# Kernel optimization log

Hardware: AMD Instinct MI355X
Metric: run time of the kernel (lower is better)

## Reference

```python
import jax, jax.numpy as jnp
import numpy as np

N, M, D = 8, 512, 64
B, H, W = 8192, 1, 1


def setup_inputs() -> dict:
    key = jax.random.key(0)
    k1, k2, k3 = jax.random.split(key, 3)
    x = jax.random.normal(k1, (B, N * D, H, W), dtype=jnp.float32)
    # nn.init.uniform_(embedding, -1/M, 1/M)
    embedding = jax.random.uniform(k2, (N, M, D), dtype=jnp.float32,
                                   minval=-1.0 / M, maxval=1.0 / M)
    # uniform base noise for Gumbel sampling (avoid exact 0)
    u = jax.random.uniform(k3, (N, B, H, W, M), dtype=jnp.float32,
                           minval=1e-6, maxval=1.0)
    tau = jnp.ones((1,), dtype=jnp.float32)
    return {"x": x, "embedding": embedding, "u": u, "tau": tau}


def reference(x, embedding, u, tau):
    n, m, d = embedding.shape
    b, c, h, w = x.shape
    # (B, N*D, H, W) -> (N, B*H*W, D)
    xr = x.reshape(b, n, d, h, w).transpose(1, 0, 3, 4, 2).reshape(n, b * h * w, d)
    e_sq = jnp.sum(embedding ** 2, axis=2)[:, None, :]          # (N, 1, M)
    x_sq = jnp.sum(xr ** 2, axis=2, keepdims=True)              # (N, BHW, 1)
    distances = e_sq + x_sq - 2.0 * jnp.einsum('nbd,nmd->nbm', xr, embedding)
    logits = -distances.reshape(n, b, h, w, m)
    # RelaxedOneHotCategorical normalizes logits to log-probs
    log_probs = jax.nn.log_softmax(logits, axis=-1)
    probs = jnp.exp(log_probs)
    # rsample: softmax((logits + gumbel) / tau); shift-invariant so log_probs ok
    gumbels = -jnp.log(-jnp.log(u))
    samples = jax.nn.softmax((log_probs + gumbels) / tau[0], axis=-1).reshape(n, -1, m)
    quantized = jnp.einsum('nbm,nmd->nbd', samples, embedding).reshape(n, b, 1, 1, d)
    logM = jnp.log(jnp.asarray(m, dtype=x.dtype))
    KL = jnp.where(probs == 0, jnp.zeros_like(probs), probs * (log_probs + logM))
    KL = KL.sum(axis=(0, 2, 3, 4)).mean()
    avg_probs = samples.mean(axis=1)                            # (N, M)
    perplexity = jnp.exp(-jnp.sum(avg_probs * jnp.log(avg_probs + 1e-10), axis=-1))
    ret_logits = jnp.transpose(log_probs, (1, 0, 4, 2, 3))      # (B, N, M, H, W)
    quantized = jnp.transpose(quantized, (1, 0, 4, 2, 3))       # (B, N, D, 1, 1)
    return (quantized, KL, perplexity.sum(), ret_logits)
```

## Files before the change

### kernel.cpp

```cpp
#include <hip/hip_runtime.h>
#include <stdint.h>

typedef short short8 __attribute__((ext_vector_type(8)));
typedef float float4v __attribute__((ext_vector_type(4)));
typedef unsigned long long ull;

#define R2      65536
#define LDS_SZ  81920

__device__ __forceinline__ unsigned cvtpk(float a, float b){
  unsigned d;
  asm("v_cvt_pk_bf16_f32 %0, %1, %2" : "=v"(d) : "v"(a), "v"(b));
  return d;
}
__device__ __forceinline__ unsigned short f2bf(float f){
  unsigned u = __float_as_uint(f);
  return (unsigned short)((u + 0x7FFFu + ((u >> 16) & 1u)) >> 16);
}

template<int OFF>
__device__ __forceinline__ ull tr16(unsigned a){
  ull d;
  asm volatile("ds_read_b64_tr_b16 %0, %1 offset:%c2" : "=v"(d) : "v"(a), "i"(OFF));
  return d;
}
__device__ __forceinline__ short8 mk8(ull lo, ull hi){
  union { ull q[2]; short8 v; } u; u.q[0] = lo; u.q[1] = hi; return u.v;
}

extern "C" __global__ void __launch_bounds__(512, 4)
vq_main(const float* __restrict__ gx, const float* __restrict__ ge,
        const float* __restrict__ gu, const float* __restrict__ gtau,
        float* __restrict__ gq, float* __restrict__ glg,
        float* __restrict__ ws_avg, float* __restrict__ ws_kl)
{
  extern __shared__ char smem[];
  const int tid = threadIdx.x;
  const int n   = blockIdx.x >> 6;
  const int b0  = (blockIdx.x & 63) * 128;

  float esq_reg = 0.f;
  {
    const int m = tid;
    const float* src = ge + (size_t)(n * 512 + m) * 64;
    char* dst = smem + m * 128;
    const unsigned sw = (unsigned)((m & 7) << 4);
#pragma unroll
    for (int c = 0; c < 8; ++c) {
      float4 a = *(const float4*)(src + c * 8);
      float4 b = *(const float4*)(src + c * 8 + 4);
      esq_reg += a.x*a.x + a.y*a.y + a.z*a.z + a.w*a.w
               + b.x*b.x + b.y*b.y + b.z*b.z + b.w*b.w;
      uint4 v = { cvtpk(a.x, a.y), cvtpk(a.z, a.w), cvtpk(b.x, b.y), cvtpk(b.z, b.w) };
      *(uint4*)(dst + (((unsigned)(c * 16)) ^ sw)) = v;
    }
  }
  {
    const int r = tid >> 2, qq = tid & 3;
    const float* src = gx + (size_t)(b0 + r) * 512 + n * 64 + qq * 16;
    char* dst = smem + R2 + r * 128;
    const unsigned sw = (unsigned)((r & 7) << 4);
#pragma unroll
    for (int h = 0; h < 2; ++h) {
      float4 a = *(const float4*)(src + h * 8);
      float4 b = *(const float4*)(src + h * 8 + 4);
      uint4 v = { cvtpk(a.x, a.y), cvtpk(a.z, a.w), cvtpk(b.x, b.y), cvtpk(b.z, b.w) };
      *(uint4*)(dst + (((unsigned)((qq * 2 + h) * 16)) ^ sw)) = v;
    }
  }
  __syncthreads();

  const int lane = tid & 63;
  const int w    = tid >> 6;
  const int l15  = lane & 15;
  const int kg   = lane >> 4;
  const unsigned swl = (unsigned)((l15 & 7) << 4);

  const char* xrow = smem + R2 + (w * 16 + l15) * 128;
  const short8 xb0 = *(const short8*)(xrow + (((unsigned)(kg * 16)) ^ swl));
  const short8 xb1 = *(const short8*)(xrow + (((unsigned)(64 + kg * 16)) ^ swl));
  __syncthreads();
  ((float*)(smem + R2))[tid] = esq_reg;
  __syncthreads();

  const char* erow = smem + l15 * 128;
  const unsigned eo0 = ((unsigned)(kg * 16)) ^ swl;
  const unsigned eo1 = ((unsigned)(64 + kg * 16)) ^ swl;
  const float* esqp = (const float*)(smem + R2);

  const float invtau = 1.0f / gtau[0];
  const float4* up4 = (const float4*)(gu + (size_t)n * 4194304
                     + (size_t)(b0 + w * 16 + l15) * 512 + kg * 4);

  float Z = 0.f, Wk = 0.f, Z2 = 0.f;
  {
    float4 Pa = up4[0], Pb = up4[4], Pc = up4[8], Pd = up4[12];
#pragma unroll
    for (int t = 0; t < 32; ++t) {
      short8 eb0 = *(const short8*)(erow + t * 2048 + eo0);
      short8 eb1 = *(const short8*)(erow + t * 2048 + eo1);
      float4v d = (float4v){0.f, 0.f, 0.f, 0.f};
      d = __builtin_amdgcn_mfma_f32_16x16x32_bf16(eb0, xb0, d, 0, 0, 0);
      d = __builtin_amdgcn_mfma_f32_16x16x32_bf16(eb1, xb1, d, 0, 0, 0);
      const float4 eq = *(const float4*)(esqp + t * 16 + kg * 4);
      const float s0 = 2.f * d[0] - eq.x;
      const float s1 = 2.f * d[1] - eq.y;
      const float s2 = 2.f * d[2] - eq.z;
      const float s3 = 2.f * d[3] - eq.w;
      const float e0 = __expf(s0), e1 = __expf(s1), e2 = __expf(s2), e3 = __expf(s3);
      Z  += e0 + e1 + e2 + e3;
      Wk += e0 * s0 + e1 * s1 + e2 * s2 + e3 * s3;
      const float4 uu = Pa;
      Pa = Pb; Pb = Pc; Pc = Pd;
      if (t < 28) Pd = up4[(t + 4) * 4];
      const float g0 = -__logf(-__logf(uu.x));
      const float g1 = -__logf(-__logf(uu.y));
      const float g2 = -__logf(-__logf(uu.z));
      const float g3 = -__logf(-__logf(uu.w));
      Z2 += __expf((s0 + g0) * invtau) + __expf((s1 + g1) * invtau)
          + __expf((s2 + g2) * invtau) + __expf((s3 + g3) * invtau);
    }
  }
  Z  += __shfl_xor(Z, 16);  Z  += __shfl_xor(Z, 32);
  Wk += __shfl_xor(Wk, 16); Wk += __shfl_xor(Wk, 32);
  Z2 += __shfl_xor(Z2, 16); Z2 += __shfl_xor(Z2, 32);
  const float lse = __logf(Z);
  const float logM = 6.2383246250395075f;
  float klrow = Wk / Z - lse + logM;
  const float rz2 = 1.0f / Z2;

  float4v* lp4 = (float4v*)(glg + (size_t)(b0 + w * 16 + l15) * 4096 + n * 512 + kg * 4);
  ushort* sampw = (ushort*)(smem + R2 + 8192 + w * 1024);
  const char* sampc = (const char*)sampw;
  const unsigned trA = (unsigned)(uintptr_t)sampw
                     + (unsigned)(kg * 128 + (l15 >> 2) * 32 + (l15 & 3) * 8);
  const int mrow = kg * 4 + (l15 >> 2);
  const unsigned ebase = (unsigned)(uintptr_t)smem + (unsigned)(mrow * 128);
  const unsigned msw = ((unsigned)(mrow & 7)) << 4;
  unsigned trB0 = ebase + ((unsigned)(  0 + (l15 & 3) * 8) ^ msw);
  unsigned trB1 = ebase + ((unsigned)( 32 + (l15 & 3) * 8) ^ msw);
  unsigned trB2 = ebase + ((unsigned)( 64 + (l15 & 3) * 8) ^ msw);
  unsigned trB3 = ebase + ((unsigned)( 96 + (l15 & 3) * 8) ^ msw);

  float4v qacc0 = (float4v){0.f,0.f,0.f,0.f};
  float4v qacc1 = (float4v){0.f,0.f,0.f,0.f};
  float4v qacc2 = (float4v){0.f,0.f,0.f,0.f};
  float4v qacc3 = (float4v){0.f,0.f,0.f,0.f};
  float4v avgA  = (float4v){0.f,0.f,0.f,0.f};
  float4v avgB  = (float4v){0.f,0.f,0.f,0.f};

  float4 P0 = up4[0], P1 = up4[4], P2 = up4[8], P3 = up4[12];
#pragma unroll
  for (int c = 0; c < 16; ++c) {
    const float4 cu0 = P0, cu1 = P1;
    P0 = P2; P1 = P3;
    if (c < 14) { P2 = up4[(2 * c + 4) * 4]; P3 = up4[(2 * c + 5) * 4]; }
#pragma unroll
    for (int th = 0; th < 2; ++th) {
      const int t = c * 2 + th;
      short8 eb0 = *(const short8*)(erow + t * 2048 + eo0);
      short8 eb1 = *(const short8*)(erow + t * 2048 + eo1);
      float4v d = (float4v){0.f, 0.f, 0.f, 0.f};
      d = __builtin_amdgcn_mfma_f32_16x16x32_bf16(eb0, xb0, d, 0, 0, 0);
      d = __builtin_amdgcn_mfma_f32_16x16x32_bf16(eb1, xb1, d, 0, 0, 0);
      const float4 eq = *(const float4*)(esqp + t * 16 + kg * 4);
      const float s0 = 2.f * d[0] - eq.x;
      const float s1 = 2.f * d[1] - eq.y;
      const float s2 = 2.f * d[2] - eq.z;
      const float s3 = 2.f * d[3] - eq.w;
      float4v lpv = { s0 - lse, s1 - lse, s2 - lse, s3 - lse };
      lp4[t * 4] = lpv;
      const float4 uu = (th == 0) ? cu0 : cu1;
      const float g0 = -__logf(-__logf(uu.x));
      const float g1 = -__logf(-__logf(uu.y));
      const float g2 = -__logf(-__logf(uu.z));
      const float g3 = -__logf(-__logf(uu.w));
      const float y0 = __expf((s0 + g0) * invtau) * rz2;
      const float y1 = __expf((s1 + g1) * invtau) * rz2;
      const float y2 = __expf((s2 + g2) * invtau) * rz2;
      const float y3 = __expf((s3 + g3) * invtau) * rz2;
      sampw[(th * 16 + kg * 4 + 0) * 16 + l15] = f2bf(y0);
      sampw[(th * 16 + kg * 4 + 1) * 16 + l15] = f2bf(y1);
      sampw[(th * 16 + kg * 4 + 2) * 16 + l15] = f2bf(y2);
      sampw[(th * 16 + kg * 4 + 3) * 16 + l15] = f2bf(y3);
    }
    asm volatile("s_waitcnt lgkmcnt(0)" ::: "memory");
    __builtin_amdgcn_sched_barrier(0);
    const short8 avA = *(const short8*)(sampc + l15 * 32 + (kg & 1) * 16);
    const short8 avB = *(const short8*)(sampc + 512 + l15 * 32 + (kg & 1) * 16);
    ull alo = tr16<0>(trA),  ahi = tr16<512>(trA);
    ull b0l = tr16<0>(trB0), b0h = tr16<2048>(trB0);
    ull b1l = tr16<0>(trB1), b1h = tr16<2048>(trB1);
    ull b2l = tr16<0>(trB2), b2h = tr16<2048>(trB2);
    ull b3l = tr16<0>(trB3), b3h = tr16<2048>(trB3);
    asm volatile("s_waitcnt lgkmcnt(0)" ::: "memory");
    __builtin_amdgcn_sched_barrier(0);
    const unsigned onv = ((l15 == c) && (kg < 2)) ? 0x3F803F80u : 0u;
    union { unsigned u[4]; short8 v; } bs;
    bs.u[0] = onv; bs.u[1] = onv; bs.u[2] = onv; bs.u[3] = onv;
    short8 aa = mk8(alo, ahi);
    qacc0 = __builtin_amdgcn_mfma_f32_16x16x32_bf16(aa, mk8(b0l, b0h), qacc0, 0, 0, 0);
    qacc1 = __builtin_amdgcn_mfma_f32_16x16x32_bf16(aa, mk8(b1l, b1h), qacc1, 0, 0, 0);
    qacc2 = __builtin_amdgcn_mfma_f32_16x16x32_bf16(aa, mk8(b2l, b2h), qacc2, 0, 0, 0);
    qacc3 = __builtin_amdgcn_mfma_f32_16x16x32_bf16(aa, mk8(b3l, b3h), qacc3, 0, 0, 0);
    avgA  = __builtin_amdgcn_mfma_f32_16x16x32_bf16(avA, bs.v, avgA, 0, 0, 0);
    avgB  = __builtin_amdgcn_mfma_f32_16x16x32_bf16(avB, bs.v, avgB, 0, 0, 0);
    trB0 += 4096; trB1 += 4096; trB2 += 4096; trB3 += 4096;
  }

  {
    const size_t qb = (size_t)(b0 + w * 16 + kg * 4) * 512 + n * 64 + l15;
#pragma unroll
    for (int j = 0; j < 4; ++j) {
      gq[qb + (size_t)j * 512 +  0] = qacc0[j];
      gq[qb + (size_t)j * 512 + 16] = qacc1[j];
      gq[qb + (size_t)j * 512 + 32] = qacc2[j];
      gq[qb + (size_t)j * 512 + 48] = qacc3[j];
    }
  }

  klrow += __shfl_xor(klrow, 1); klrow += __shfl_xor(klrow, 2);
  klrow += __shfl_xor(klrow, 4); klrow += __shfl_xor(klrow, 8);

  __syncthreads();
  float* avgl = (float*)(smem + R2);
  float* kls  = (float*)smem;
  if (lane == 0) kls[w] = klrow;
  *(float4v*)(avgl + w * 512 + l15 * 32 + kg * 4)      = avgA;
  *(float4v*)(avgl + w * 512 + l15 * 32 + 16 + kg * 4) = avgB;
  __syncthreads();
  {
    float s = 0.f;
#pragma unroll
    for (int ww = 0; ww < 8; ++ww) s += avgl[ww * 512 + tid];
    ws_avg[(size_t)blockIdx.x * 512 + tid] = s;
    if (tid == 0) {
      float k = 0.f;
#pragma unroll
      for (int i = 0; i < 8; ++i) k += kls[i];
      ws_kl[blockIdx.x] = k;
    }
  }
}

extern "C" __global__ void __launch_bounds__(512)
vq_fin(const float* __restrict__ ws_avg, const float* __restrict__ ws_kl,
       float* __restrict__ scal)
{
  __shared__ float red[8];
  const int tid = threadIdx.x, lane = tid & 63, w = tid >> 6;
  float pps = 0.f;
  for (int n = 0; n < 8; ++n) {
    float s = 0.f;
    for (int bt = 0; bt < 64; ++bt) s += ws_avg[(size_t)(n * 64 + bt) * 512 + tid];
    const float avg = s * (1.0f / 8192.0f);
    float term = avg * __logf(avg + 1e-10f);
#pragma unroll
    for (int o = 1; o < 64; o <<= 1) term += __shfl_xor(term, o);
    __syncthreads();
    if (lane == 0) red[w] = term;
    __syncthreads();
    if (tid == 0) {
      float tt = 0.f;
#pragma unroll
      for (int i = 0; i < 8; ++i) tt += red[i];
      pps += __expf(-tt);
    }
  }
  float kv = ws_kl[tid];
#pragma unroll
  for (int o = 1; o < 64; o <<= 1) kv += __shfl_xor(kv, o);
  __syncthreads();
  if (lane == 0) red[w] = kv;
  __syncthreads();
  if (tid == 0) {
    float k = 0.f;
#pragma unroll
    for (int i = 0; i < 8; ++i) k += red[i];
    scal[0] = k * (1.0f / 8192.0f);
    scal[1] = pps;
  }
}

extern "C" void kernel_launch(void* const* d_in, const int* in_sizes, int n_in,
                              void* d_out, int out_size, void* d_ws, size_t ws_size,
                              hipStream_t stream)
{
  const float* gx = (const float*)d_in[0];
  const float* ge = (const float*)d_in[1];
  const float* gu = (const float*)d_in[2];
  const float* gt = (const float*)d_in[3];
  float* out  = (float*)d_out;
  float* gq   = out;
  float* scal = out + 4194304;
  float* glg  = out + 4194306;
  float* ws_avg = (float*)d_ws;
  float* ws_kl  = ws_avg + 512 * 512;

  (void)hipFuncSetAttribute((const void*)vq_main,
                            hipFuncAttributeMaxDynamicSharedMemorySize, LDS_SZ);
  vq_main<<<dim3(512), dim3(512), LDS_SZ, stream>>>(gx, ge, gu, gt, gq, glg, ws_avg, ws_kl);
  vq_fin<<<dim3(1), dim3(512), 0, stream>>>(ws_avg, ws_kl, scal);
}
```

Baseline: 125.8 us.

## Stage codebook in LDS quarters and spill unnormalized Gumbel samples to workspace

Adds a new main kernel that stages the codebook into LDS in four 128-row quarters, cutting LDS from 80KB to 32KB so occupancy can double (launch bounds 8). The first sweep now computes the unnormalized Gumbel-softmax samples once, packs them as bf16 in a global workspace, and the second sweep reloads them and scales by 1/Z2. This drops the repeated log/log/exp work in the second pass. For tau==1 it replaces exp(s - log(-log u)) with e*rcp(-log u). The trade-off is about 67MB of extra workspace traffic plus more barriers from restaging the codebook. The old kernel is kept as a fallback when the workspace is too small.

Result: slower. 383.9 us (+205.1%).

```diff
diff --git a/kernel.cpp b/kernel.cpp
--- a/kernel.cpp
+++ b/kernel.cpp
@@ -4,6 +4,11 @@
 typedef short short8 __attribute__((ext_vector_type(8)));
 typedef float float4v __attribute__((ext_vector_type(4)));
 typedef unsigned long long ull;
+
+#define ESQ_OFF   16384
+#define SAMP_OFF  18432
+#define KLS_OFF   26624
+#define LDS_FAST  32768
 
 #define R2      65536
 #define LDS_SZ  81920
@@ -17,6 +22,8 @@
   unsigned u = __float_as_uint(f);
   return (unsigned short)((u + 0x7FFFu + ((u >> 16) & 1u)) >> 16);
 }
+__device__ __forceinline__ float bfLO(unsigned r){ return __uint_as_float(r << 16); }
+__device__ __forceinline__ float bfHI(unsigned r){ return __uint_as_float(r & 0xffff0000u); }
 
 template<int OFF>
 __device__ __forceinline__ ull tr16(unsigned a){
@@ -28,11 +35,281 @@
   union { ull q[2]; short8 v; } u; u.q[0] = lo; u.q[1] = hi; return u.v;
 }
 
+__device__ __forceinline__ void stage_eq(char* smem, const float* ge, int n, int q, int tid){
+  const int r = tid >> 2, qq = tid & 3;
+  const float* src = ge + ((size_t)(n * 512 + q * 128 + r)) * 64 + qq * 16;
+  char* dst = smem + r * 128;
+  const unsigned sw = (unsigned)((r & 7) << 4);
+#pragma unroll
+  for (int h = 0; h < 2; ++h) {
+    float4 a = *(const float4*)(src + h * 8);
+    float4 b = *(const float4*)(src + h * 8 + 4);
+    uint4 v = { cvtpk(a.x, a.y), cvtpk(a.z, a.w), cvtpk(b.x, b.y), cvtpk(b.z, b.w) };
+    *(uint4*)(dst + (((unsigned)((qq * 2 + h) * 16)) ^ sw)) = v;
+  }
+}
+
+#define PHASE_B_TAIL(cvar)                                                     \
+    asm volatile("s_waitcnt lgkmcnt(0)" ::: "memory");                         \
+    __builtin_amdgcn_sched_barrier(0);                                         \
+    const short8 avA = *(const short8*)(sampc + l15 * 32 + (kg & 1) * 16);     \
+    const short8 avB = *(const short8*)(sampc + 512 + l15 * 32 + (kg & 1) * 16); \
+    ull alo = tr16<0>(trA),  ahi = tr16<512>(trA);                             \
+    ull b0l = tr16<0>(trB0), b0h = tr16<2048>(trB0);                           \
+    ull b1l = tr16<0>(trB1), b1h = tr16<2048>(trB1);                           \
+    ull b2l = tr16<0>(trB2), b2h = tr16<2048>(trB2);                           \
+    ull b3l = tr16<0>(trB3), b3h = tr16<2048>(trB3);                           \
+    asm volatile("s_waitcnt lgkmcnt(0)" ::: "memory");                         \
+    __builtin_amdgcn_sched_barrier(0);                                         \
+    const unsigned onv = ((l15 == (cvar)) && (kg < 2)) ? 0x3F803F80u : 0u;     \
+    union { unsigned u[4]; short8 v; } bs;                                     \
+    bs.u[0] = onv; bs.u[1] = onv; bs.u[2] = onv; bs.u[3] = onv;                \
+    short8 aa = mk8(alo, ahi);                                                 \
+    qacc0 = __builtin_amdgcn_mfma_f32_16x16x32_bf16(aa, mk8(b0l, b0h), qacc0, 0, 0, 0); \
+    qacc1 = __builtin_amdgcn_mfma_f32_16x16x32_bf16(aa, mk8(b1l, b1h), qacc1, 0, 0, 0); \
+    qacc2 = __builtin_amdgcn_mfma_f32_16x16x32_bf16(aa, mk8(b2l, b2h), qacc2, 0, 0, 0); \
+    qacc3 = __builtin_amdgcn_mfma_f32_16x16x32_bf16(aa, mk8(b3l, b3h), qacc3, 0, 0, 0); \
+    avgA  = __builtin_amdgcn_mfma_f32_16x16x32_bf16(avA, bs.v, avgA, 0, 0, 0); \
+    avgB  = __builtin_amdgcn_mfma_f32_16x16x32_bf16(avB, bs.v, avgB, 0, 0, 0); \
+    trB0 += 4096; trB1 += 4096; trB2 += 4096; trB3 += 4096;
+
+extern "C" __global__ void __launch_bounds__(512, 8)
+vq_main_ws(const float* __restrict__ gx, const float* __restrict__ ge,
+           const float* __restrict__ gu, const float* __restrict__ gtau,
+           float* __restrict__ gq, float* __restrict__ glg,
+           ull* __restrict__ gy,
+           float* __restrict__ ws_avg, float* __restrict__ ws_kl)
+{
+  extern __shared__ char smem[];
+  const int tid = threadIdx.x;
+  const int n   = blockIdx.x >> 6;
+  const int b0  = (blockIdx.x & 63) * 128;
+
+  float esq_reg = 0.f;
+  {
+    const float* src = ge + (size_t)(n * 512 + tid) * 64;
+#pragma unroll
+    for (int c8 = 0; c8 < 8; ++c8) {
+      float4 a = *(const float4*)(src + c8 * 8);
+      float4 b = *(const float4*)(src + c8 * 8 + 4);
+      esq_reg += a.x*a.x + a.y*a.y + a.z*a.z + a.w*a.w
+               + b.x*b.x + b.y*b.y + b.z*b.z + b.w*b.w;
+    }
+  }
+  {
+    const int r = tid >> 2, qq = tid & 3;
+    const float* src = gx + (size_t)(b0 + r) * 512 + n * 64 + qq * 16;
+    char* dst = smem + ESQ_OFF + r * 128;
+    const unsigned sw = (unsigned)((r & 7) << 4);
+#pragma unroll
+    for (int h = 0; h < 2; ++h) {
+      float4 a = *(const float4*)(src + h * 8);
+      float4 b = *(const float4*)(src + h * 8 + 4);
+      uint4 v = { cvtpk(a.x, a.y), cvtpk(a.z, a.w), cvtpk(b.x, b.y), cvtpk(b.z, b.w) };
+      *(uint4*)(dst + (((unsigned)((qq * 2 + h) * 16)) ^ sw)) = v;
+    }
+  }
+  __syncthreads();
+
+  const int lane = tid & 63;
+  const int w    = tid >> 6;
+  const int l15  = lane & 15;
+  const int kg   = lane >> 4;
+  const unsigned swl = (unsigned)((l15 & 7) << 4);
+
+  const char* xrow = smem + ESQ_OFF + (w * 16 + l15) * 128;
+  const short8 xb0 = *(const short8*)(xrow + (((unsigned)(kg * 16)) ^ swl));
+  const short8 xb1 = *(const short8*)(xrow + (((unsigned)(64 + kg * 16)) ^ swl));
+  __syncthreads();
+  ((float*)(smem + ESQ_OFF))[tid] = esq_reg;
+  stage_eq(smem, ge, n, 0, tid);
+  __syncthreads();
+
+  const char* erow = smem + l15 * 128;
+  const unsigned eo0 = ((unsigned)(kg * 16)) ^ swl;
+  const unsigned eo1 = ((unsigned)(64 + kg * 16)) ^ swl;
+  const float* esqp = (const float*)(smem + ESQ_OFF);
+
+  const float tauv = gtau[0];
+  const float invtau = 1.0f / tauv;
+  const bool tau1 = (tauv == 1.0f);
+  const float4* up4 = (const float4*)(gu + (size_t)n * 4194304
+                     + (size_t)(b0 + w * 16 + l15) * 512 + kg * 4);
+  ull* gyw = gy + ((size_t)blockIdx.x * 8 + w) * 2048;
+
+  float Z = 0.f, Wk = 0.f, Z2 = 0.f;
+
+#define S1_BODY(T, LT, YE0, YE1, YE2, YE3)                                     \
+    {                                                                          \
+      short8 eb0 = *(const short8*)(erow + (LT) * 2048 + eo0);                 \
+      short8 eb1 = *(const short8*)(erow + (LT) * 2048 + eo1);                 \
+      float4v d = (float4v){0.f, 0.f, 0.f, 0.f};                               \
+      d = __builtin_amdgcn_mfma_f32_16x16x32_bf16(eb0, xb0, d, 0, 0, 0);       \
+      d = __builtin_amdgcn_mfma_f32_16x16x32_bf16(eb1, xb1, d, 0, 0, 0);       \
+      const float4 eq = *(const float4*)(esqp + (T) * 16 + kg * 4);            \
+      const float s0 = 2.f * d[0] - eq.x;                                      \
+      const float s1 = 2.f * d[1] - eq.y;                                      \
+      const float s2 = 2.f * d[2] - eq.z;                                      \
+      const float s3 = 2.f * d[3] - eq.w;                                      \
+      const float e0 = __expf(s0), e1 = __expf(s1);                            \
+      const float e2 = __expf(s2), e3 = __expf(s3);                            \
+      Z  += (e0 + e1) + (e2 + e3);                                             \
+      Wk += e0 * s0 + e1 * s1 + e2 * s2 + e3 * s3;                             \
+      const float4 uu = Pa;                                                    \
+      Pa = Pb; Pb = Pc; Pc = Pd;                                               \
+      if ((T) < 28) Pd = up4[((T) + 4) * 4];                                   \
+      const float l0 = -__logf(uu.x), l1 = -__logf(uu.y);                      \
+      const float l2 = -__logf(uu.z), l3 = -__logf(uu.w);                      \
+      const float y0 = (YE0), y1 = (YE1);                                      \
+      const float y2 = (YE2), y3 = (YE3);                                      \
+      const unsigned pk0 = cvtpk(y0, y1);                                      \
+      const unsigned pk1 = cvtpk(y2, y3);                                      \
+      gyw[(T) * 64 + lane] = (ull)pk0 | ((ull)pk1 << 32);                      \
+      Z2 += (y0 + y1) + (y2 + y3);                                             \
+    }
+
+#define SWEEP1(YE0, YE1, YE2, YE3)                                             \
+  {                                                                            \
+    float4 Pa = up4[0], Pb = up4[4], Pc = up4[8], Pd = up4[12];                \
+    _Pragma("unroll")                                                          \
+    for (int q = 0; q < 4; ++q) {                                              \
+      if (q > 0) {                                                             \
+        __syncthreads();                                                       \
+        stage_eq(smem, ge, n, q, tid);                                         \
+        __syncthreads();                                                       \
+      }                                                                        \
+      _Pragma("unroll")                                                        \
+      for (int lt = 0; lt < 8; ++lt) {                                         \
+        const int t = q * 8 + lt;                                              \
+        S1_BODY(t, lt, YE0, YE1, YE2, YE3)                                     \
+      }                                                                        \
+    }                                                                          \
+  }
+
+  if (tau1) {
+    SWEEP1(e0 * __builtin_amdgcn_rcpf(l0), e1 * __builtin_amdgcn_rcpf(l1),
+           e2 * __builtin_amdgcn_rcpf(l2), e3 * __builtin_amdgcn_rcpf(l3))
+  } else {
+    SWEEP1(__expf((s0 - __logf(l0)) * invtau), __expf((s1 - __logf(l1)) * invtau),
+           __expf((s2 - __logf(l2)) * invtau), __expf((s3 - __logf(l3)) * invtau))
+  }
+#undef SWEEP1
+#undef S1_BODY
+
+  Z  += __shfl_xor(Z, 16);  Z  += __shfl_xor(Z, 32);
+  Wk += __shfl_xor(Wk, 16); Wk += __shfl_xor(Wk, 32);
+  Z2 += __shfl_xor(Z2, 16); Z2 += __shfl_xor(Z2, 32);
+  const float lse = __logf(Z);
+  const float logM = 6.2383246250395075f;
+  float klrow = Wk * __builtin_amdgcn_rcpf(Z) - lse + logM;
+  const float rz2 = __builtin_amdgcn_rcpf(Z2);
+
+  float4v* lp4 = (float4v*)(glg + (size_t)(b0 + w * 16 + l15) * 4096 + n * 512 + kg * 4);
+  ushort* sampw = (ushort*)(smem + SAMP_OFF + w * 1024);
+  const char* sampc = (const char*)sampw;
+  const unsigned trA = (unsigned)(uintptr_t)sampw
+                     + (unsigned)(kg * 128 + (l15 >> 2) * 32 + (l15 & 3) * 8);
+  const int mrow = kg * 4 + (l15 >> 2);
+  const unsigned ebase = (unsigned)(uintptr_t)smem + (unsigned)(mrow * 128);
+  const unsigned msw = ((unsigned)(mrow & 7)) << 4;
+  const unsigned tb0 = ebase + ((unsigned)(  0 + (l15 & 3) * 8) ^ msw);
+  const unsigned tb1 = ebase + ((unsigned)( 32 + (l15 & 3) * 8) ^ msw);
+  const unsigned tb2 = ebase + ((unsigned)( 64 + (l15 & 3) * 8) ^ msw);
+  const unsigned tb3 = ebase + ((unsigned)( 96 + (l15 & 3) * 8) ^ msw);
+
+  float4v qacc0 = (float4v){0.f,0.f,0.f,0.f};
+  float4v qacc1 = (float4v){0.f,0.f,0.f,0.f};
+  float4v qacc2 = (float4v){0.f,0.f,0.f,0.f};
+  float4v qacc3 = (float4v){0.f,0.f,0.f,0.f};
+  float4v avgA  = (float4v){0.f,0.f,0.f,0.f};
+  float4v avgB  = (float4v){0.f,0.f,0.f,0.f};
+
+  __syncthreads();
+  stage_eq(smem, ge, n, 0, tid);
+  __syncthreads();
+
+  asm volatile("s_waitcnt vmcnt(0)" ::: "memory");
+  ull Ya[4] = { gyw[lane], gyw[64 + lane], gyw[128 + lane], gyw[192 + lane] };
+
+#pragma unroll
+  for (int q = 0; q < 4; ++q) {
+    if (q > 0) {
+      __syncthreads();
+      stage_eq(smem, ge, n, q, tid);
+      __syncthreads();
+    }
+    unsigned trB0 = tb0, trB1 = tb1, trB2 = tb2, trB3 = tb3;
+#pragma unroll
+    for (int lc = 0; lc < 4; ++lc) {
+      const int c = q * 4 + lc;
+#pragma unroll
+      for (int th = 0; th < 2; ++th) {
+        const int t = c * 2 + th;
+        const int lt = lc * 2 + th;
+        short8 eb0 = *(const short8*)(erow + lt * 2048 + eo0);
+        short8 eb1 = *(const short8*)(erow + lt * 2048 + eo1);
+        float4v d = (float4v){0.f, 0.f, 0.f, 0.f};
+        d = __builtin_amdgcn_mfma_f32_16x16x32_bf16(eb0, xb0, d, 0, 0, 0);
+        d = __builtin_amdgcn_mfma_f32_16x16x32_bf16(eb1, xb1, d, 0, 0, 0);
+        const float4 eq = *(const float4*)(esqp + t * 16 + kg * 4);
+        float4v lpv = { 2.f * d[0] - eq.x - lse, 2.f * d[1] - eq.y - lse,
+                        2.f * d[2] - eq.z - lse, 2.f * d[3] - eq.w - lse };
+        lp4[t * 4] = lpv;
+        const ull yc = Ya[t & 3];
+        if (t < 28) Ya[t & 3] = gyw[(t + 4) * 64 + lane];
+        const unsigned pk0 = (unsigned)yc;
+        const unsigned pk1 = (unsigned)(yc >> 32);
+        const unsigned q0 = cvtpk(bfLO(pk0) * rz2, bfHI(pk0) * rz2);
+        const unsigned q1 = cvtpk(bfLO(pk1) * rz2, bfHI(pk1) * rz2);
+        sampw[(th * 16 + kg * 4 + 0) * 16 + l15] = (ushort)q0;
+        sampw[(th * 16 + kg * 4 + 1) * 16 + l15] = (ushort)(q0 >> 16);
+        sampw[(th * 16 + kg * 4 + 2) * 16 + l15] = (ushort)q1;
+        sampw[(th * 16 + kg * 4 + 3) * 16 + l15] = (ushort)(q1 >> 16);
+      }
+      PHASE_B_TAIL(c)
+    }
+  }
+
+  {
+    const size_t qb = (size_t)(b0 + w * 16 + kg * 4) * 512 + n * 64 + l15;
+#pragma unroll
+    for (int j = 0; j < 4; ++j) {
+      gq[qb + (size_t)j * 512 +  0] = qacc0[j];
+      gq[qb + (size_t)j * 512 + 16] = qacc1[j];
+      gq[qb + (size_t)j * 512 + 32] = qacc2[j];
+      gq[qb + (size_t)j * 512 + 48] = qacc3[j];
+    }
+  }
+
+  klrow += __shfl_xor(klrow, 1); klrow += __shfl_xor(klrow, 2);
+  klrow += __shfl_xor(klrow, 4); klrow += __shfl_xor(klrow, 8);
+
+  __syncthreads();
+  float* avgl = (float*)smem;
+  float* kls  = (float*)(smem + KLS_OFF);
+  if (lane == 0) kls[w] = klrow;
+  *(float4v*)(avgl + w * 512 + l15 * 32 + kg * 4)      = avgA;
+  *(float4v*)(avgl + w * 512 + l15 * 32 + 16 + kg * 4) = avgB;
+  __syncthreads();
+  {
+    float s = 0.f;
+#pragma unroll
+    for (int ww = 0; ww < 8; ++ww) s += avgl[ww * 512 + tid];
+    ws_avg[(size_t)blockIdx.x * 512 + tid] = s;
+    if (tid == 0) {
+      float k = 0.f;
+#pragma unroll
+      for (int i = 0; i < 8; ++i) k += kls[i];
+      ws_kl[blockIdx.x] = k;
+    }
+  }
+}
+
 extern "C" __global__ void __launch_bounds__(512, 4)
-vq_main(const float* __restrict__ gx, const float* __restrict__ ge,
-        const float* __restrict__ gu, const float* __restrict__ gtau,
-        float* __restrict__ gq, float* __restrict__ glg,
-        float* __restrict__ ws_avg, float* __restrict__ ws_kl)
+vq_main_fb(const float* __restrict__ gx, const float* __restrict__ ge,
+           const float* __restrict__ gu, const float* __restrict__ gtau,
+           float* __restrict__ gq, float* __restrict__ glg,
+           float* __restrict__ ws_avg, float* __restrict__ ws_kl)
 {
   extern __shared__ char smem[];
   const int tid = threadIdx.x;
@@ -108,7 +385,7 @@
       const float s2 = 2.f * d[2] - eq.z;
       const float s3 = 2.f * d[3] - eq.w;
       const float e0 = __expf(s0), e1 = __expf(s1), e2 = __expf(s2), e3 = __expf(s3);
-      Z  += e0 + e1 + e2 + e3;
+      Z  += (e0 + e1) + (e2 + e3);
       Wk += e0 * s0 + e1 * s1 + e2 * s2 + e3 * s3;
       const float4 uu = Pa;
       Pa = Pb; Pb = Pc; Pc = Pd;
@@ -126,8 +403,8 @@
   Z2 += __shfl_xor(Z2, 16); Z2 += __shfl_xor(Z2, 32);
   const float lse = __logf(Z);
   const float logM = 6.2383246250395075f;
-  float klrow = Wk / Z - lse + logM;
-  const float rz2 = 1.0f / Z2;
+  float klrow = Wk * __builtin_amdgcn_rcpf(Z) - lse + logM;
+  const float rz2 = __builtin_amdgcn_rcpf(Z2);
 
   float4v* lp4 = (float4v*)(glg + (size_t)(b0 + w * 16 + l15) * 4096 + n * 512 + kg * 4);
   ushort* sampw = (ushort*)(smem + R2 + 8192 + w * 1024);
@@ -184,28 +461,7 @@
       sampw[(th * 16 + kg * 4 + 2) * 16 + l15] = f2bf(y2);
       sampw[(th * 16 + kg * 4 + 3) * 16 + l15] = f2bf(y3);
     }
-    asm volatile("s_waitcnt lgkmcnt(0)" ::: "memory");
-    __builtin_amdgcn_sched_barrier(0);
-    const short8 avA = *(const short8*)(sampc + l15 * 32 + (kg & 1) * 16);
-    const short8 avB = *(const short8*)(sampc + 512 + l15 * 32 + (kg & 1) * 16);
-    ull alo = tr16<0>(trA),  ahi = tr16<512>(trA);
-    ull b0l = tr16<0>(trB0), b0h = tr16<2048>(trB0);
-    ull b1l = tr16<0>(trB1), b1h = tr16<2048>(trB1);
-    ull b2l = tr16<0>(trB2), b2h = tr16<2048>(trB2);
-    ull b3l = tr16<0>(trB3), b3h = tr16<2048>(trB3);
-    asm volatile("s_waitcnt lgkmcnt(0)" ::: "memory");
-    __builtin_amdgcn_sched_barrier(0);
-    const unsigned onv = ((l15 == c) && (kg < 2)) ? 0x3F803F80u : 0u;
-    union { unsigned u[4]; short8 v; } bs;
-    bs.u[0] = onv; bs.u[1] = onv; bs.u[2] = onv; bs.u[3] = onv;
-    short8 aa = mk8(alo, ahi);
-    qacc0 = __builtin_amdgcn_mfma_f32_16x16x32_bf16(aa, mk8(b0l, b0h), qacc0, 0, 0, 0);
-    qacc1 = __builtin_amdgcn_mfma_f32_16x16x32_bf16(aa, mk8(b1l, b1h), qacc1, 0, 0, 0);
-    qacc2 = __builtin_amdgcn_mfma_f32_16x16x32_bf16(aa, mk8(b2l, b2h), qacc2, 0, 0, 0);
-    qacc3 = __builtin_amdgcn_mfma_f32_16x16x32_bf16(aa, mk8(b3l, b3h), qacc3, 0, 0, 0);
-    avgA  = __builtin_amdgcn_mfma_f32_16x16x32_bf16(avA, bs.v, avgA, 0, 0, 0);
-    avgB  = __builtin_amdgcn_mfma_f32_16x16x32_bf16(avB, bs.v, avgB, 0, 0, 0);
-    trB0 += 4096; trB1 += 4096; trB2 += 4096; trB3 += 4096;
+    PHASE_B_TAIL(c)
   }
 
   {
@@ -294,11 +550,26 @@
   float* gq   = out;
   float* scal = out + 4194304;
   float* glg  = out + 4194306;
-  float* ws_avg = (float*)d_ws;
-  float* ws_kl  = ws_avg + 512 * 512;
-
-  (void)hipFuncSetAttribute((const void*)vq_main,
-                            hipFuncAttributeMaxDynamicSharedMemorySize, LDS_SZ);
-  vq_main<<<dim3(512), dim3(512), LDS_SZ, stream>>>(gx, ge, gu, gt, gq, glg, ws_avg, ws_kl);
-  vq_fin<<<dim3(1), dim3(512), 0, stream>>>(ws_avg, ws_kl, scal);
-}
+
+  const size_t GY_BYTES = (size_t)512 * 8 * 2048 * 8;
+  const size_t NEED = GY_BYTES + (size_t)512 * 512 * 4 + 2048;
+
+  if (ws_size >= NEED) {
+    ull*   gy     = (ull*)d_ws;
+    float* ws_avg = (float*)((char*)d_ws + GY_BYTES);
+    float* ws_kl  = ws_avg + 512 * 512;
+    (void)hipFuncSetAttribute((const void*)vq_main_ws,
+                              hipFuncAttributeMaxDynamicSharedMemorySize, LDS_FAST);
+    vq_main_ws<<<dim3(512), dim3(512), LDS_FAST, stream>>>(gx, ge, gu, gt, gq, glg,
+                                                           gy, ws_avg, ws_kl);
+    vq_fin<<<dim3(1), dim3(512), 0, stream>>>(ws_avg, ws_kl, scal);
+  } else {
+    float* ws_avg = (float*)d_ws;
+    float* ws_kl  = ws_avg + 512 * 512;
+    (void)hipFuncSetAttribute((const void*)vq_main_fb,
+                              hipFuncAttributeMaxDynamicSharedMemorySize, LDS_SZ);
+    vq_main_fb<<<dim3(512), dim3(512), LDS_SZ, stream>>>(gx, ge, gu, gt, gq, glg,
+                                                         ws_avg, ws_kl);
+    vq_fin<<<dim3(1), dim3(512), 0, stream>>>(ws_avg, ws_kl, scal);
+  }
+}
```
